# Performance work log

Measured on AMD Instinct MI355X. Metric: run time of the kernel, lower is better.

## Reference

```python
import jax, jax.numpy as jnp
import numpy as np
from jax import lax

# ---- fake-quant helpers (brevitas-style per-tensor float scaling, STE round) ----
EPS = 1e-8

def _ste_round(x):
    return x + lax.stop_gradient(jnp.round(x) - x)

def _scale(x, qmax):
    s = lax.stop_gradient(jnp.max(jnp.abs(x))) / qmax
    return jnp.maximum(s, EPS)

def fq(x, scale, qmin, qmax):
    # fake-quantize: round-to-nearest with straight-through estimator, clip, dequant
    return jnp.clip(_ste_round(x / scale), qmin, qmax) * scale

def quant_act_int8(x):
    s = _scale(x, 127.0)
    return fq(x, s, -128.0, 127.0), s

def quant_weight_int4(w):
    # 4-bit signed, narrow range [-7, 7] (brevitas weight quant default narrow_range)
    s = _scale(w, 7.0)
    return fq(w, s, -7.0, 7.0), s

def quant_relu_uint4(x):
    y = jax.nn.relu(x)
    s = _scale(y, 15.0)
    return fq(y, s, 0.0, 15.0)

def quant_bias_int32(b, scale):
    # Int32Bias: bias quantized at input_scale * weight_scale
    return _ste_round(b / scale) * scale

def conv2d_same(x, w):
    # NCHW, OIHW, padding=1, stride=1
    return lax.conv_general_dilated(x, w, window_strides=(1, 1), padding=((1, 1), (1, 1)),
                                    dimension_numbers=('NCHW', 'OIHW', 'NCHW'))

def maxpool2(x):
    return lax.reduce_window(x, -jnp.inf, lax.max, (1, 1, 2, 2), (1, 1, 2, 2), 'VALID')

def quant_conv(x, w, b):
    xq, sx = quant_act_int8(x)        # input_quant: Int8ActPerTensorFloat
    wq, sw = quant_weight_int4(w)     # weight_bit_width=4
    bq = quant_bias_int32(b, sx * sw) # bias_quant: Int32Bias
    y = conv2d_same(xq, wq) + bq[None, :, None, None]
    yq, _ = quant_act_int8(y)         # output_quant: Int8ActPerTensorFloat
    return yq

def quant_linear(x, w, b):
    xq, sx = quant_act_int8(x)
    wq, sw = quant_weight_int4(w)
    bq = quant_bias_int32(b, sx * sw)
    y = xq @ wq.T + bq
    yq, _ = quant_act_int8(y)
    return yq


def setup_inputs() -> dict:
    key = jax.random.key(0)
    ks = jax.random.split(key, 7)
    B = 8192
    x = jax.random.normal(ks[0], (B, 1, 28, 28), dtype=jnp.float32)
    w1 = jax.random.normal(ks[1], (16, 1, 3, 3), dtype=jnp.float32) * 0.3
    b1 = jax.random.normal(ks[2], (16,), dtype=jnp.float32) * 0.1
    w2 = jax.random.normal(ks[3], (32, 16, 3, 3), dtype=jnp.float32) * 0.1
    b2 = jax.random.normal(ks[4], (32,), dtype=jnp.float32) * 0.1
    wf = jax.random.normal(ks[5], (10, 32 * 7 * 7), dtype=jnp.float32) * 0.05
    bf = jax.random.normal(ks[6], (10,), dtype=jnp.float32) * 0.1
    return {'x': x, 'w1': w1, 'b1': b1, 'w2': w2, 'b2': b2, 'wf': wf, 'bf': bf}


def reference(x, w1, b1, w2, b2, wf, bf):
    h, _ = quant_act_int8(x)              # inputQuant
    h = quant_conv(h, w1, b1)             # conv1
    h = quant_relu_uint4(h)               # relu1 (4-bit)
    h = maxpool2(h)                       # pool1 -> [B,16,14,14]
    h = quant_conv(h, w2, b2)             # conv2
    h = quant_relu_uint4(h)               # relu2
    h = maxpool2(h)                       # pool2 -> [B,32,7,7]
    h = h.reshape(h.shape[0], -1)         # flatten -> [B,1568]
    return quant_linear(h, wf, bf)        # fc -> [B,10]
```

## Files before the change

### kernel.cpp

```cpp
#include <hip/hip_runtime.h>
#include <climits>

#define NB 8192
#define EPSQ 1e-8f

using i32x4  = __attribute__((ext_vector_type(4)))  int;
using i32x16 = __attribute__((ext_vector_type(16))) int;

#define WS_F(ws)     ((float*)(ws))
#define WS_I(ws)     ((int*)((char*)(ws)+128))
#define WS_B1L(ws)   ((int*)((char*)(ws)+384))
#define WS_B2L(ws)   ((int*)((char*)(ws)+448))
#define WS_BFL(ws)   ((int*)((char*)(ws)+576))
#define WS_M1F(ws)   ((float*)((char*)(ws)+640))
#define WS_B1F(ws)   ((float*)((char*)(ws)+1280))
#define WS_W1P(ws)   ((unsigned*)((char*)(ws)+1408))
#define WS_B2FR(ws)  ((char*)(ws)+2048)
#define WS_Q2TAB(ws) ((signed char*)((char*)(ws)+7168))
#define WS_Q3TAB(ws) ((signed char*)((char*)(ws)+7424))
#define WS_B1FR(ws)  ((char*)(ws)+7680)
#define WS_MFF(ws)   ((float*)((char*)(ws)+20480))
#define WS_WFP(ws)   ((char*)(ws)+83200)
#define WS_RA1(ws)   ((int*)((char*)(ws)+139264))
#define WS_RS1(ws)   ((int*)((char*)(ws)+164352))
#define WS_RA2(ws)   ((int*)((char*)(ws)+189440))
#define WS_RS2(ws)   ((int*)((char*)(ws)+197632))
#define WS_RA3(ws)   ((int*)((char*)(ws)+205824))
#define WS_RAX(ws)   ((float*)((char*)(ws)+206848))
#define WS_WMX(ws)   ((float*)((char*)(ws)+215040))
#define WS_Q2B(ws)   ((signed char*)((char*)(ws)+215552))
#define WS_BIG_OFF   281600

__device__ __forceinline__ float clampf(float v, float lo, float hi){ return fminf(fmaxf(v, lo), hi); }

__device__ __forceinline__ int dot4(unsigned a, unsigned b, int c){
  return __builtin_amdgcn_sdot4((int)a, (int)b, c, false);
}

__device__ __forceinline__ float wave_max_f(float v){
#pragma unroll
  for (int off=32; off; off>>=1) v = fmaxf(v, __shfl_down(v, off, 64));
  return v;
}
__device__ __forceinline__ int wave_max_i(int v){
#pragma unroll
  for (int off=32; off; off>>=1) v = max(v, __shfl_down(v, off, 64));
  return v;
}

__device__ __forceinline__ void reduce2_atomic(int amax, int smax, int* gA, int* gS){
  amax = wave_max_i(amax); smax = wave_max_i(smax);
  __shared__ int sA[4], sS[4];
  int w = threadIdx.x>>6, l = threadIdx.x&63;
  if (l==0){ sA[w]=amax; sS[w]=smax; }
  __syncthreads();
  if (threadIdx.x==0){
#pragma unroll
    for (int i=1;i<4;i++){ amax=max(amax,sA[i]); smax=max(smax,sS[i]); }
    atomicMax(gA, amax); atomicMax(gS, smax);
  }
}

__device__ __forceinline__ void reduce2_store(int amax, int smax, int* pA, int* pS){
  amax = wave_max_i(amax); smax = wave_max_i(smax);
  __shared__ int sA[4], sS[4];
  int w = threadIdx.x>>6, l = threadIdx.x&63;
  if (l==0){ sA[w]=amax; sS[w]=smax; }
  __syncthreads();
  if (threadIdx.x==0){
#pragma unroll
    for (int i=1;i<4;i++){ amax=max(amax,sA[i]); smax=max(smax,sS[i]); }
    *pA = amax; *pS = smax;
  }
}

__global__ void k_init(char* ws){
  int* I = WS_I(ws);
  if (threadIdx.x==0){ I[0]=0; I[1]=0; I[2]=INT_MIN; I[3]=0; I[4]=INT_MIN; I[5]=0; }
}

__global__ void k_absx(const float* __restrict__ x, char* ws){
  const float4* x4 = (const float4*)x;
  const int n4 = NB*784/4;
  float m = 0.f;
  for (int i = blockIdx.x*blockDim.x + threadIdx.x; i < n4; i += gridDim.x*blockDim.x){
    float4 v = x4[i];
    m = fmaxf(m, fmaxf(fmaxf(fabsf(v.x),fabsf(v.y)), fmaxf(fabsf(v.z),fabsf(v.w))));
  }
  m = wave_max_f(m);
  __shared__ float sm[4];
  int w = threadIdx.x>>6;
  if ((threadIdx.x&63)==0) sm[w]=m;
  __syncthreads();
  if (threadIdx.x==0){
    m = fmaxf(fmaxf(sm[0],sm[1]), fmaxf(sm[2],sm[3]));
    WS_RAX(ws)[blockIdx.x] = m;
  }
}

__global__ void k_absxw(const float* __restrict__ x,
                        const float* __restrict__ w1, const float* __restrict__ w2,
                        const float* __restrict__ wf, char* ws){
  __shared__ float red[256];
  int b = blockIdx.x, t = threadIdx.x;
  if (b < 81){
    float m = 0.f;
    if (b==0){ if (t<144) m = fabsf(w1[t]); }
    else if (b<19){ m = fabsf(w2[(b-1)*256 + t]); }
    else { int i=(b-19)*256+t; if (i<15680) m = fabsf(wf[i]); }
    red[t]=m; __syncthreads();
    for (int s=128;s;s>>=1){ if (t<s) red[t]=fmaxf(red[t],red[t+s]); __syncthreads(); }
    if (t==0) WS_WMX(ws)[b]=red[0];
    return;
  }
  const int xb = b - 81;
  const float4* x4 = (const float4*)x;
  const int n4 = NB*784/4;
  float m = 0.f;
  for (int i = xb*256 + t; i < n4; i += 2048*256){
    float4 v = x4[i];
    m = fmaxf(m, fmaxf(fmaxf(fabsf(v.x),fabsf(v.y)), fmaxf(fabsf(v.z),fabsf(v.w))));
  }
  m = wave_max_f(m);
  __shared__ float sm[4];
  int w = t>>6;
  if ((t&63)==0) sm[w]=m;
  __syncthreads();
  if (t==0){
    m = fmaxf(fmaxf(sm[0],sm[1]), fmaxf(sm[2],sm[3]));
    WS_RAX(ws)[xb] = m;
  }
}

__global__ void k_scales(const float* __restrict__ w1, const float* __restrict__ b1, char* ws){
  __shared__ float red[256];
  float* F = WS_F(ws);
  int t = threadIdx.x;
  float vw1 = WS_WMX(ws)[0];
  float m2=0.f, mf=0.f;
  if (t<18) m2 = WS_WMX(ws)[1+t];
  if (t<62) mf = WS_WMX(ws)[19+t];
  red[t]=m2; __syncthreads();
  for (int s=128;s;s>>=1){ if (t<s) red[t]=fmaxf(red[t],red[t+s]); __syncthreads(); }
  float mw2=red[0]; __syncthreads();
  red[t]=mf; __syncthreads();
  for (int s=128;s;s>>=1){ if (t<s) red[t]=fmaxf(red[t],red[t+s]); __syncthreads(); }
  float mwf=red[0]; __syncthreads();
  float mxv=0.f;
  for (int i=t;i<2048;i+=256) mxv=fmaxf(mxv,WS_RAX(ws)[i]);
  red[t]=mxv; __syncthreads();
  for (int s=128;s;s>>=1){ if (t<s) red[t]=fmaxf(red[t],red[t+s]); __syncthreads(); }
  float mx=red[0]; __syncthreads();

  float s0  = fmaxf(mx/127.f, EPSQ);
  float sx1 = fmaxf((127.f*s0)/127.f, EPSQ);
  float sw1 = fmaxf(vw1/7.f, EPSQ);
  float sw2 = fmaxf(mw2/7.f, EPSQ);
  float swf = fmaxf(mwf/7.f, EPSQ);
  float sb1 = sx1*sw1;
  if (t==0){ F[0]=s0; F[1]=sx1; F[2]=sw1; F[3]=sb1; F[7]=sw2; F[12]=swf; }
  if (t<144) WS_M1F(ws)[t] = clampf(rintf(w1[t]/sw1), -7.f, 7.f);
  if (t<16){
    int bl = (int)rintf(b1[t]/sb1);
    WS_B1L(ws)[t] = bl;
    WS_B1F(ws)[t] = (float)bl;
  }
  __syncthreads();
  if (t<48){
    int oc = t/3, row = t - oc*3;
    const float* m = WS_M1F(ws) + oc*9 + row*3;
    unsigned b0 = (unsigned)(unsigned char)(signed char)(int)m[0];
    unsigned bb1 = (unsigned)(unsigned char)(signed char)(int)m[1];
    unsigned b2c = (unsigned)(unsigned char)(signed char)(int)m[2];
    WS_W1P(ws)[t] = b0 | (bb1<<8) | (b2c<<16);
  }
}

__global__ void k_pack(const float* __restrict__ w1, const float* __restrict__ w2,
                       const float* __restrict__ wf, char* ws){
  const float* F = WS_F(ws);
  int id = blockIdx.x*256 + threadIdx.x;
  if (id < 5120){
    float sw2 = F[7];
    int chunk=id>>10, r=id&1023, ln=r>>4, j=r&15;
    int tap=2*chunk+(ln>>5), oc=ln&31;
    signed char v=0;
    if (tap<9) v=(signed char)clampf(rintf(w2[oc*144 + j*9 + tap]/sw2), -7.f, 7.f);
    WS_B2FR(ws)[id]=v;
  } else if (id < 6144){
    float sw1 = F[2];
    int i=id-5120;
    int ln=i>>4, j=i&15;
    int k=(ln>>5)*16+j, oc=ln&31;
    signed char v=0;
    if (k<9 && oc<16) v=(signed char)clampf(rintf(w1[oc*9+k]/sw1), -7.f, 7.f);
    WS_B1FR(ws)[i]=v;
  } else if (id < 56320){
    float swf = F[12];
    int i=id-6144;
    int chunk=i>>10, r2=i&1023, ln=r2>>4, j=r2&15;
    int oc=ln&31, k=chunk*32+(ln>>5)*16+j;
    int cell=k>>5, ch=k&31;
    signed char v=0;
    if (oc<10) v=(signed char)clampf(rintf(wf[oc*1568 + ch*49 + cell]/swf), -7.f, 7.f);
    ((signed char*)WS_WFP(ws))[i]=v;
  } else if (id < 72000){
    float swf = F[12];
    int i=id-56320;
    WS_MFF(ws)[i] = clampf(rintf(wf[i]/swf), -7.f, 7.f);
  }
}

__global__ void k_wq(const float* __restrict__ w1, const float* __restrict__ b1,
                     const float* __restrict__ w2, const float* __restrict__ wf,
                     char* ws){
  __shared__ float red[256];
  float* F = WS_F(ws);
  int t = threadIdx.x;
  auto bmaxabs = [&](const float* p, int n)->float{
    float m=0.f; for (int i=t;i<n;i+=256) m=fmaxf(m,fabsf(p[i]));
    red[t]=m; __syncthreads();
    for (int s=128;s;s>>=1){ if (t<s) red[t]=fmaxf(red[t],red[t+s]); __syncthreads(); }
    float r=red[0]; __syncthreads(); return r;
  };
  float mw1 = bmaxabs(w1,144);
  float mw2 = bmaxabs(w2,4608);
  float mwf = bmaxabs(wf,15680);
  float mxv=0.f;
  for (int i=t;i<2048;i+=256) mxv=fmaxf(mxv,WS_RAX(ws)[i]);
  red[t]=mxv; __syncthreads();
  for (int s=128;s;s>>=1){ if (t<s) red[t]=fmaxf(red[t],red[t+s]); __syncthreads(); }
  float mx=red[0]; __syncthreads();

  float s0  = fmaxf(mx/127.f, EPSQ);
  float sx1 = fmaxf((127.f*s0)/127.f, EPSQ);
  float sw1 = fmaxf(mw1/7.f, EPSQ);
  float sw2 = fmaxf(mw2/7.f, EPSQ);
  float swf = fmaxf(mwf/7.f, EPSQ);
  float sb1 = sx1*sw1;
  if (t==0){ F[0]=s0; F[1]=sx1; F[2]=sw1; F[3]=sb1; F[7]=sw2; F[12]=swf; }
  float* m1f = WS_M1F(ws);
  for (int i=t;i<144;i+=256) m1f[i] = clampf(rintf(w1[i]/sw1), -7.f, 7.f);
  if (t<16){
    int bl = (int)rintf(b1[t]/sb1);
    WS_B1L(ws)[t] = bl;
    WS_B1F(ws)[t] = (float)bl;
  }
  for (int i=t;i<5120;i+=256){
    int chunk=i>>10, r=i&1023, ln=r>>4, j=r&15;
    int tap=2*chunk+(ln>>5), oc=ln&31;
    signed char v=0;
    if (tap<9) v=(signed char)clampf(rintf(w2[oc*144 + j*9 + tap]/sw2), -7.f, 7.f);
    WS_B2FR(ws)[i]=v;
  }
  for (int i=t;i<1024;i+=256){
    int ln=i>>4, j=i&15;
    int k=(ln>>5)*16+j, oc=ln&31;
    signed char v=0;
    if (k<9 && oc<16) v=(signed char)clampf(rintf(w1[oc*9+k]/sw1), -7.f, 7.f);
    WS_B1FR(ws)[i]=v;
  }
  float* mff = WS_MFF(ws);
  for (int i=t;i<15680;i+=256) mff[i] = clampf(rintf(wf[i]/swf), -7.f, 7.f);
  for (int i=t;i<50176;i+=256){
    int chunk=i>>10, r2=i&1023, ln=r2>>4, j=r2&15;
    int oc=ln&31, k=chunk*32+(ln>>5)*16+j;
    int cell=k>>5, ch=k&31;
    signed char v=0;
    if (oc<10) v=(signed char)clampf(rintf(wf[oc*1568 + ch*49 + cell]/swf), -7.f, 7.f);
    ((signed char*)WS_WFP(ws))[i]=v;
  }
}

template<bool FULLR>
__global__ void k_s1(const float* __restrict__ b2, char* ws){
  float* F=WS_F(ws); int* I=WS_I(ws);
  __shared__ int rA[256], rS[256];
  __shared__ float sh[4];
  int t=threadIdx.x;
  int amaxI, smaxI;
  if constexpr (FULLR){
    int a=0, s=INT_MIN;
    const int* ra=WS_RA1(ws); const int* rs=WS_RS1(ws);
    for (int i=t;i<6272;i+=256){ a=max(a,ra[i]); s=max(s,rs[i]); }
    rA[t]=a; rS[t]=s; __syncthreads();
    for (int st=128;st;st>>=1){ if (t<st){ rA[t]=max(rA[t],rA[t+st]); rS[t]=max(rS[t],rS[t+st]); } __syncthreads(); }
    amaxI=rA[0]; smaxI=rS[0];
  } else { amaxI=I[1]; smaxI=I[2]; }
  if (t==0){
    float sb1=F[3];
    float sy1 = fmaxf((sb1*(float)amaxI)/127.f, EPSQ);
    float mp  = sb1*(float)smaxI;
    float P1  = clampf(rintf(mp/sy1), 0.f, 127.f);
    float sr1 = fmaxf((sy1*P1)/15.f, EPSQ);
    float N1  = clampf(rintf((sy1*P1)/sr1), 0.f, 15.f);
    float sx2 = fmaxf((N1*sr1)/127.f, EPSQ);
    float sb2 = sx2*F[7];
    F[4]=sy1; F[5]=sr1; F[6]=sx2; F[8]=sb2;
    sh[0]=sy1; sh[1]=sr1; sh[2]=sx2; sh[3]=sb2;
  }
  __syncthreads();
  float sy1=sh[0], sr1=sh[1], sx2=sh[2], sb2=sh[3];
  int k = t-128;
  float n = (k>0) ? clampf(rintf((sy1*(float)k)/sr1), 0.f, 15.f) : 0.f;
  WS_Q2TAB(ws)[t] = (signed char)clampf(rintf((n*sr1)/sx2), -128.f, 127.f);
  if (t<32) WS_B2L(ws)[t] = (int)rintf(b2[t]/sb2);
}

__global__ void k_s1q2(const float* __restrict__ b2, char* ws){
  float* F=WS_F(ws);
  __shared__ int rA[256], rS[256];
  int t=threadIdx.x;
  int a=0, s=INT_MIN;
  const int* ra=WS_RA1(ws); const int* rs=WS_RS1(ws);
  for (int i=t;i<6272;i+=256){ a=max(a,ra[i]); s=max(s,rs[i]); }
  rA[t]=a; rS[t]=s; __syncthreads();
  for (int st=128;st;st>>=1){ if (t<st){ rA[t]=max(rA[t],rA[t+st]); rS[t]=max(rS[t],rS[t+st]); } __syncthreads(); }
  int amaxI=rA[0], smaxI=rS[0];
  float sb1=F[3];
  float sy1 = fmaxf((sb1*(float)amaxI)/127.f, EPSQ);
  float P1  = clampf(rintf((sb1*(float)smaxI)/sy1), 0.f, 127.f);
  float sr1 = fmaxf((sy1*P1)/15.f, EPSQ);
  float N1  = clampf(rintf((sy1*P1)/sr1), 0.f, 15.f);
  float sx2 = fmaxf((N1*sr1)/127.f, EPSQ);
  float sb2 = sx2*F[7];
  if (blockIdx.x==0){
    if (t==0){ F[4]=sy1; F[5]=sr1; F[6]=sx2; F[8]=sb2; }
    if (t<32) WS_B2L(ws)[t] = (int)rintf(b2[t]/sb2);
  }
  int idx = blockIdx.x*256 + t;
  int m = idx - 32768;
  float k1 = clampf(rintf((sb1*(float)m)/sy1), -128.f, 127.f);
  float n  = (k1>0.f) ? clampf(rintf((sy1*k1)/sr1), 0.f, 15.f) : 0.f;
  WS_Q2B(ws)[idx] = (signed char)clampf(rintf((n*sr1)/sx2), -128.f, 127.f);
}

template<bool FULLR>
__global__ void k_s2(const float* __restrict__ bf, char* ws){
  float* F=WS_F(ws); int* I=WS_I(ws);
  __shared__ int rA[256], rS[256];
  __shared__ float sh[4];
  int t=threadIdx.x;
  int amaxI, smaxI;
  if constexpr (FULLR){
    int a=0, s=INT_MIN;
    const int* ra=WS_RA2(ws); const int* rs=WS_RS2(ws);
    for (int i=t;i<2048;i+=256){ a=max(a,ra[i]); s=max(s,rs[i]); }
    rA[t]=a; rS[t]=s; __syncthreads();
    for (int st=128;st;st>>=1){ if (t<st){ rA[t]=max(rA[t],rA[t+st]); rS[t]=max(rS[t],rS[t+st]); } __syncthreads(); }
    amaxI=rA[0]; smaxI=rS[0];
  } else { amaxI=I[3]; smaxI=I[4]; }
  if (t==0){
    float sb2=F[8];
    float sy2 = fmaxf((sb2*(float)amaxI)/127.f, EPSQ);
    float mp  = sb2*(float)smaxI;
    float P2  = clampf(rintf(mp/sy2), 0.f, 127.f);
    float sr2 = fmaxf((sy2*P2)/15.f, EPSQ);
    float N2  = clampf(rintf((sy2*P2)/sr2), 0.f, 15.f);
    float sx3 = fmaxf((N2*sr2)/127.f, EPSQ);
    float sb3 = sx3*F[12];
    F[9]=sy2; F[10]=sr2; F[11]=sx3; F[13]=sb3;
    sh[0]=sy2; sh[1]=sr2; sh[2]=sx3; sh[3]=sb3;
  }
  __syncthreads();
  float sy2=sh[0], sr2=sh[1], sx3=sh[2], sb3=sh[3];
  int k = t-128;
  float n = (k>0) ? clampf(rintf((sy2*(float)k)/sr2), 0.f, 15.f) : 0.f;
  WS_Q3TAB(ws)[t] = (signed char)clampf(rintf((n*sr2)/sx3), -128.f, 127.f);
  if (t<16) WS_BFL(ws)[t] = (t<10) ? (int)rintf(bf[t]/sb3) : 0;
}

template<bool FULLR>
__global__ void k_s3(char* ws){
  float* F=WS_F(ws); int* I=WS_I(ws);
  __shared__ int rA[256];
  int t=threadIdx.x;
  int amaxI;
  if constexpr (FULLR){
    rA[t] = WS_RA3(ws)[t];
    __syncthreads();
    for (int st=128;st;st>>=1){ if (t<st) rA[t]=max(rA[t],rA[t+st]); __syncthreads(); }
    amaxI = rA[0];
  } else { amaxI = I[5]; }
  if (t==0) F[14] = fmaxf((F[13]*(float)amaxI)/127.f, EPSQ);
}

__global__ void k_qx(const float* __restrict__ x, const char* __restrict__ ws,
                     signed char* __restrict__ qx){
  const float s0 = ((const float*)ws)[0];
  int id = blockIdx.x*256 + threadIdx.x;
  int img = id/240, w = id - img*240;
  int r = w>>3, c4 = (w&7)<<2;
  const float* xi = x + img*784;
  unsigned out = 0;
#pragma unroll
  for (int j=0;j<4;j++){
    int c = c4+j;
    bool valid = (r>=1) && (r<=28) && (c>=1) && (c<=28);
    int q = 0;
    if (valid){
      float xv = xi[(r-1)*28 + (c-1)];
      q = (int)clampf(rintf(xv/s0), -128.f, 127.f);
    }
    out |= ((unsigned)(unsigned char)(signed char)q) << (8*j);
  }
  ((unsigned*)qx)[id] = out;
}

__global__ __launch_bounds__(256) void k_conv1d(const signed char* __restrict__ qx,
                                                char* __restrict__ ws,
                                                short* __restrict__ i1p){
  const int t = threadIdx.x;
  const int id = blockIdx.x*256 + t;
  const int img = id/196, cell = id - img*196;
  const int py = cell/14, px = cell - py*14;
  const signed char* qb = qx + img*960 + (2*py)*32;
  const int pc0 = 2*px;
  const int al = pc0 & ~3, sh = (pc0&3)*8;
  unsigned wrd[4], whi[4];
#pragma unroll
  for (int rr=0; rr<4; rr++){
    unsigned lo = *(const unsigned*)(qb + rr*32 + al);
    unsigned hi = *(const unsigned*)(qb + rr*32 + al + 4);
    wrd[rr] = (unsigned)(((((unsigned long long)hi)<<32)|lo) >> sh);
    whi[rr] = wrd[rr] >> 8;
  }
  const unsigned* __restrict__ w1p = WS_W1P(ws);
  const int* __restrict__ b1l = WS_B1L(ws);
  int amax=0, smax=INT_MIN;
  short outv[16];
#pragma unroll
  for (int oc=0; oc<16; oc++){
    unsigned w0 = w1p[oc*3], w1 = w1p[oc*3+1], w2 = w1p[oc*3+2];
    int bl = b1l[oc];
    int a00 = dot4(wrd[2], w2, dot4(wrd[1], w1, dot4(wrd[0], w0, bl)));
    int a01 = dot4(whi[2], w2, dot4(whi[1], w1, dot4(whi[0], w0, bl)));
    int a10 = dot4(wrd[3], w2, dot4(wrd[2], w1, dot4(wrd[1], w0, bl)));
    int a11 = dot4(whi[3], w2, dot4(whi[2], w1, dot4(whi[1], w0, bl)));
    int mx = max(max(a00,a01), max(a10,a11));
    int ax = max(max(a00<0?-a00:a00, a01<0?-a01:a01), max(a10<0?-a10:a10, a11<0?-a11:a11));
    amax = max(amax, ax);
    smax = max(smax, mx);
    outv[oc] = (short)mx;
  }
  int4* dst = (int4*)(i1p + (size_t)id*16);
  dst[0] = *(const int4*)&outv[0];
  dst[1] = *(const int4*)&outv[8];
  reduce2_store(amax, smax, &WS_RA1(ws)[blockIdx.x], &WS_RS1(ws)[blockIdx.x]);
}

__global__ __launch_bounds__(256) void k_conv2r(char* __restrict__ ws,
                                                short* __restrict__ i1p,
                                                int* __restrict__ p2g){
  __shared__ __align__(16) signed char q2p4[4][4096];
  const int t=threadIdx.x, lane=t&63, wid=t>>6;
  const int img = blockIdx.x*4 + wid;
  signed char* q2p = q2p4[wid];
  const signed char* __restrict__ q2b = WS_Q2B(ws);

#pragma unroll
  for (int k=0;k<8;k++) ((unsigned long long*)q2p)[lane + 64*k] = 0ULL;

  const unsigned* src = (const unsigned*)(i1p + (size_t)img*3136);
#pragma unroll
  for (int k=0;k<24;k++){
    int idx = lane + 64*k;
    unsigned wv = src[idx];
    int e0 = idx*2;
    int cellc = e0 >> 4, ch = e0 & 15;
    int pyc = cellc/14, pxc = cellc - pyc*14;
    int m0 = (int)(short)(wv & 0xFFFFu);
    int m1 = (int)(short)(wv >> 16);
    int b0 = (int)(unsigned char)q2b[m0+32768];
    int b1 = (int)(unsigned char)q2b[m1+32768];
    *(unsigned short*)(q2p + ((pyc+1)*16 + (pxc+1))*16 + ch) = (unsigned short)(b0 | (b1<<8));
  }
  if (lane < 32){
    int idx = 1536 + lane;
    unsigned wv = src[idx];
    int e0 = idx*2;
    int cellc = e0 >> 4, ch = e0 & 15;
    int pyc = cellc/14, pxc = cellc - pyc*14;
    int m0 = (int)(short)(wv & 0xFFFFu);
    int m1 = (int)(short)(wv >> 16);
    int b0 = (int)(unsigned char)q2b[m0+32768];
    int b1 = (int)(unsigned char)q2b[m1+32768];
    *(unsigned short*)(q2p + ((pyc+1)*16 + (pxc+1))*16 + ch) = (unsigned short)(b0 | (b1<<8));
  }

  i32x4 bfr[5];
  const i32x4* bg = (const i32x4*)WS_B2FR(ws);
#pragma unroll
  for (int c=0;c<5;c++) bfr[c] = bg[c*64+lane];
  const int col = lane&31, h = lane>>5;
  const int bias = WS_B2L(ws)[col];
  int amax2=0, smax2=INT_MIN;
  const int TOFF[9] = {0,1,2,16,17,18,32,33,34};
  int* dstb = p2g + (size_t)img*1568;

#pragma unroll
  for (int mt=0; mt<7; mt++){
    int m = mt*32 + col;
    int g = m>>2, sub = m&3;
    bool gv = g < 49;
    int py = (g*37)>>8;
    int px = g - py*7;
    int oy = 2*py + (sub>>1), ox = 2*px + (sub&1);
    int E0 = oy*16 + ox;
    i32x16 acc;
#pragma unroll
    for (int r=0;r<16;r++) acc[r] = bias;
#pragma unroll
    for (int c=0;c<5;c++){
      const int t0 = TOFF[2*c];
      const int t1 = (2*c+1<9) ? TOFF[2*c+1] : -1;
      int toff = h ? t1 : t0;
      int entry = (gv && toff>=0) ? (E0 + toff) : 0;
      i32x4 a = *(const i32x4*)(q2p + entry*16);
      acc = __builtin_amdgcn_mfma_i32_32x32x32_i8(a, bfr[c], acc, 0,0,0);
    }
#pragma unroll
    for (int i=0;i<4;i++){
      int gg = mt*8 + 2*i + h;
      if (gg < 49){
        int v0=acc[4*i], v1=acc[4*i+1], v2=acc[4*i+2], v3=acc[4*i+3];
        int a0=v0<0?-v0:v0, a1=v1<0?-v1:v1, a2=v2<0?-v2:v2, a3=v3<0?-v3:v3;
        amax2 = max(amax2, max(max(a0,a1),max(a2,a3)));
        int mx = max(max(v0,v1),max(v2,v3));
        smax2 = max(smax2, mx);
        dstb[gg*32 + col] = mx;
      }
    }
  }
  reduce2_store(amax2, smax2, &WS_RA2(ws)[blockIdx.x], &WS_RS2(ws)[blockIdx.x]);
}

__global__ void k_rq2(const char* __restrict__ ws, const int* __restrict__ p2g,
                      signed char* __restrict__ q3g){
  const float* F = (const float*)ws;
  const float sb2 = F[8], sy2 = F[9];
  const signed char* q3t = WS_Q3TAB(ws);
  int id = blockIdx.x*256 + threadIdx.x;
  i32x4 m4 = ((const i32x4*)p2g)[id];
  unsigned out=0;
#pragma unroll
  for (int j=0;j<4;j++){
    float k2 = clampf(rintf((sb2*(float)m4[j])/sy2), -128.f, 127.f);
    out |= ((unsigned)(unsigned char)q3t[(int)k2+128]) << (8*j);
  }
  ((unsigned*)q3g)[id] = out;
}

__global__ __launch_bounds__(256) void k_fc(char* __restrict__ ws,
                                            const signed char* __restrict__ q3g,
                                            int* __restrict__ i3out){
  __shared__ int part[3][16][64];
  int t=threadIdx.x, lane=t&63, wid=t>>6;
  int mt = blockIdx.x;
  const int col=lane&31, h=lane>>5;
  const signed char* A0 = q3g + (size_t)(mt*32 + col)*1568 + 16*h;
  const i32x4* wfp = (const i32x4*)WS_WFP(ws);
  i32x16 acc;
#pragma unroll
  for (int r=0;r<16;r++) acc[r]=0;
#pragma unroll
  for (int cc=0; cc<13; cc++){
    int c = wid + cc*4;
    if (c < 49){
      i32x4 a = *(const i32x4*)(A0 + c*32);
      i32x4 b = wfp[c*64 + lane];
      acc = __builtin_amdgcn_mfma_i32_32x32x32_i8(a, b, acc, 0,0,0);
    }
  }
  if (wid>0){
#pragma unroll
    for (int r=0;r<16;r++) part[wid-1][r][lane] = acc[r];
  }
  __syncthreads();
  if (wid==0){
    int bias = (col<10) ? WS_BFL(ws)[col] : 0;
    int am=0;
#pragma unroll
    for (int r=0;r<16;r++){
      int v = acc[r] + part[0][r][lane] + part[1][r][lane] + part[2][r][lane] + bias;
      int row=(r&3)+8*(r>>2)+4*h;
      int img = mt*32+row;
      if (col<10){
        i3out[img*10+col] = v;
        am = max(am, v<0?-v:v);
      }
    }
    am = wave_max_i(am);
    if (lane==0) WS_RA3(ws)[blockIdx.x] = am;
  }
}

__global__ void k_out2(char* __restrict__ ws, float* __restrict__ out){
  __shared__ int rA[256];
  int t=threadIdx.x;
  rA[t] = WS_RA3(ws)[t];
  __syncthreads();
  for (int st=128;st;st>>=1){ if (t<st) rA[t]=max(rA[t],rA[t+st]); __syncthreads(); }
  float sb3 = WS_F(ws)[13];
  float sy3 = fmaxf((sb3*(float)rA[0])/127.f, EPSQ);
  int i = blockIdx.x*256 + t;
  if (i < NB*10){
    int iv = ((const int*)out)[i];
    float y = sb3*(float)iv;
    float q = clampf(rintf(y/sy3), -128.f, 127.f);
    out[i] = q*sy3;
  }
}

__global__ __launch_bounds__(256) void k_c1(const float* __restrict__ x, char* __restrict__ ws,
                                            short* __restrict__ i1p){
  constexpr int OFF_K0=0, OFF_A=960, OFF_I1=13760, OFF_B1=38848;
  __shared__ __align__(16) char arena[38912];
  signed char* k0b = (signed char*)(arena+OFF_K0);
  signed char* Abuf= (signed char*)(arena+OFF_A);
  short*       I1s = (short*)(arena+OFF_I1);
  int*         b1i = (int*)(arena+OFF_B1);

  const int tid=threadIdx.x, img=blockIdx.x;
  const int lane=tid&63, wid=tid>>6;
  const float s0 = WS_F(ws)[0];

  if (tid<16) b1i[tid]=WS_B1L(ws)[tid];
  for (int i=tid;i<240;i+=256) ((int*)k0b)[i]=0;
  for (int i=tid;i<3200;i+=256) ((int*)Abuf)[i]=0;
  __syncthreads();
  const float* xi = x + img*784;
  for (int i=tid;i<784;i+=256){
    int r=i/28, c=i-r*28;
    float v = clampf(rintf(xi[i]/s0), -128.f, 127.f);
    k0b[(r+1)*32 + (c+1)] = (signed char)v;
  }
  __syncthreads();
  for (int p=tid;p<784;p+=256){
    int oy=p/28, ox=p-oy*28;
    int base = oy*32+ox;
    int al = base & ~3, sh = (base&3)*8;
    unsigned l0a=*(const unsigned*)(k0b+al),    l1a=*(const unsigned*)(k0b+al+4);
    unsigned l0b=*(const unsigned*)(k0b+al+32), l1b=*(const unsigned*)(k0b+al+36);
    unsigned l0c=*(const unsigned*)(k0b+al+64), l1c=*(const unsigned*)(k0b+al+68);
    unsigned u0=(unsigned)(((((unsigned long long)l1a)<<32)|l0a)>>sh);
    unsigned u1=(unsigned)(((((unsigned long long)l1b)<<32)|l0b)>>sh);
    unsigned u2=(unsigned)(((((unsigned long long)l1c)<<32)|l0c)>>sh);
    i32x4 row;
    row[0]=(int)((u0&0xFFFFFFu)|(u1<<24));
    row[1]=(int)(((u1>>8)&0xFFFFu)|((u2&0xFFFFu)<<16));
    row[2]=(int)((u2>>16)&0xFFu);
    row[3]=0;
    *(i32x4*)(Abuf + p*16) = row;
  }
  __syncthreads();
  const i32x4 bfr = ((const i32x4*)WS_B1FR(ws))[lane];
  const int col=lane&31, h=lane>>5;
  const int bias=(col<16)? b1i[col] : 0;
  int amax=0, smax=INT_MIN;
  for (int mt=wid; mt<25; mt+=4){
    i32x4 a={0,0,0,0};
    if (h==0) a = *(const i32x4*)(Abuf + (mt*32+col)*16);
    i32x16 acc;
#pragma unroll
    for (int r=0;r<16;r++) acc[r]=bias;
    acc=__builtin_amdgcn_mfma_i32_32x32x32_i8(a,bfr,acc,0,0,0);
#pragma unroll
    for (int r=0;r<16;r++){
      int row=(r&3)+8*(r>>2)+4*h;
      int p=mt*32+row;
      if (p<784 && col<16){
        int v=acc[r];
        amax=max(amax,v<0?-v:v); smax=max(smax,v);
        I1s[p*16+col]=(short)v;
      }
    }
  }
  __syncthreads();
  for (int i=tid;i<3136;i+=256){
    int pp=i>>4, c=i&15, py=pp/14, px=pp-py*14;
    int p0=py*56+px*2;
    int m=max(max((int)I1s[p0*16+c],(int)I1s[(p0+1)*16+c]),
              max((int)I1s[(p0+28)*16+c],(int)I1s[(p0+29)*16+c]));
    i1p[(size_t)img*3136 + i]=(short)m;
  }
  reduce2_atomic(amax,smax,&WS_I(ws)[1],&WS_I(ws)[2]);
}

template<bool FIN>
__global__ __launch_bounds__(256) void k_c2(char* __restrict__ ws, const short* __restrict__ i1p,
                                            int* __restrict__ i3out){
  constexpr int OFF_Q2L=0, OFF_B2I=3136, OFF_Q2T=3264, OFF_N2=3520,
                OFF_Q3T=9792, OFF_BFS=10048, OFF_Q3F=10112, OFF_RED=16384;
  constexpr int ARENA = FIN ? 16544 : 3520;
  __shared__ __align__(16) char arena[ARENA];
  signed char* q2l=(signed char*)(arena+OFF_Q2L);
  int* b2li=(int*)(arena+OFF_B2I);
  signed char* q2t=(signed char*)(arena+OFF_Q2T);

  const int tid=threadIdx.x, img=blockIdx.x;
  const int lane=tid&63, wid=tid>>6;
  const float* F=WS_F(ws);
  const float sb1=F[3], sy1=F[4];

  q2t[tid]=WS_Q2TAB(ws)[tid];
  if (tid<32) b2li[tid]=WS_B2L(ws)[tid];
  if constexpr (FIN){
    ((signed char*)(arena+OFF_Q3T))[tid]=WS_Q3TAB(ws)[tid];
    if (tid<16) ((int*)(arena+OFF_BFS))[tid]=WS_BFL(ws)[tid];
  }
  __syncthreads();
  for (int i=tid;i<3136;i+=256){
    int m=(int)i1p[(size_t)img*3136+i];
    float k1=clampf(rintf((sb1*(float)m)/sy1),-128.f,127.f);
    q2l[i]=q2t[(int)k1+128];
  }
  __syncthreads();

  i32x4 bfr[5];
  {
    const i32x4* bg=(const i32x4*)WS_B2FR(ws);
#pragma unroll
    for (int c=0;c<5;c++) bfr[c]=bg[c*64+lane];
  }
  const int col=lane&31, h=lane>>5;
  const int bias=b2li[col];
  int amax2=0, smax2=INT_MIN;
  float sb2=0.f, sy2=0.f;
  signed char* n2buf=nullptr;
  if constexpr (FIN){ sb2=F[8]; sy2=F[9]; n2buf=(signed char*)(arena+OFF_N2); }

  for (int mt=wid; mt<7; mt+=4){
    const int p=mt*32+col;
    const bool pv=p<196;
    const int oy=p/14, ox=p-oy*14;
    i32x16 acc;
#pragma unroll
    for (int r=0;r<16;r++) acc[r]=bias;
#pragma unroll
    for (int c=0;c<5;c++){
      const int tap=2*c+h;
      i32x4 a={0,0,0,0};
      if (pv && tap<9){
        const int iy=oy+tap/3-1, ix=ox+tap-(tap/3)*3-1;
        if ((unsigned)iy<14u && (unsigned)ix<14u) a=*(const i32x4*)(q2l+(iy*14+ix)*16);
      }
      acc=__builtin_amdgcn_mfma_i32_32x32x32_i8(a,bfr[c],acc,0,0,0);
    }
#pragma unroll
    for (int r=0;r<16;r++){
      const int row=(r&3)+8*(r>>2)+4*h;
      const int pp=mt*32+row;
      if (pp<196){
        const int v=acc[r];
        if constexpr (!FIN){ amax2=max(amax2,v<0?-v:v); smax2=max(smax2,v); }
        else {
          n2buf[col*196+pp]=(signed char)clampf(rintf((sb2*(float)v)/sy2),-128.f,127.f);
        }
      }
    }
  }
  if constexpr (!FIN){
    reduce2_atomic(amax2,smax2,&WS_I(ws)[3],&WS_I(ws)[4]);
    return;
  } else {
    __syncthreads();
    signed char* q3t_s=(signed char*)(arena+OFF_Q3T);
    float* q3f=(float*)(arena+OFF_Q3F);
    for (int i=tid;i<1568;i+=256){
      int cch=i/49, s=i-cch*49, qy=s/7, qx=s-qy*7;
      int b=cch*196+qy*28+qx*2;
      int m=max(max((int)n2buf[b],(int)n2buf[b+1]),max((int)n2buf[b+14],(int)n2buf[b+15]));
      q3f[i]=(float)q3t_s[m+128];
    }
    __syncthreads();
    const float* mff=WS_MFF(ws);
    float a10[10];
#pragma unroll
    for (int o=0;o<10;o++) a10[o]=0.f;
    for (int k=tid;k<1568;k+=256){
      float qa=q3f[k];
#pragma unroll
      for (int o=0;o<10;o++) a10[o]=fmaf(qa,mff[o*1568+k],a10[o]);
    }
#pragma unroll
    for (int o=0;o<10;o++){
#pragma unroll
      for (int off=32;off;off>>=1) a10[o]+=__shfl_down(a10[o],off,64);
    }
    float* redf=(float*)(arena+OFF_RED);
    int* bfs=(int*)(arena+OFF_BFS);
    if (lane==0){
#pragma unroll
      for (int o=0;o<10;o++) redf[wid*10+o]=a10[o];
    }
    __syncthreads();
    if (tid<10){
      float s=redf[tid]+redf[10+tid]+redf[20+tid]+redf[30+tid];
      int I3v=(int)s+bfs[tid];
      i3out[img*10+tid]=I3v;
      redf[tid]=(float)(I3v<0?-I3v:I3v);
    }
    __syncthreads();
    if (tid==0){
      int m=0;
#pragma unroll
      for (int o=0;o<10;o++) m=max(m,(int)redf[o]);
      atomicMax(&WS_I(ws)[5],m);
    }
  }
}

__global__ void k_out(char* ws, float* __restrict__ out){
  float* F=WS_F(ws);
  float sb3=F[13], sy3=F[14];
  int i = blockIdx.x*blockDim.x + threadIdx.x;
  if (i < NB*10){
    int iv = ((const int*)out)[i];
    float y = sb3*(float)iv;
    float q = clampf(rintf(y/sy3), -128.f, 127.f);
    out[i] = q*sy3;
  }
}

extern "C" void kernel_launch(void* const* d_in, const int* in_sizes, int n_in,
                              void* d_out, int out_size, void* d_ws, size_t ws_size,
                              hipStream_t stream){
  const float* x  = (const float*)d_in[0];
  const float* w1 = (const float*)d_in[1];
  const float* b1 = (const float*)d_in[2];
  const float* w2 = (const float*)d_in[3];
  const float* b2 = (const float*)d_in[4];
  const float* wf = (const float*)d_in[5];
  const float* bf = (const float*)d_in[6];
  char* ws = (char*)d_ws;
  float* out = (float*)d_out;
  int* i3 = (int*)d_out;

  const size_t QX_SZ  = (size_t)NB*960;
  const size_t I1_SZ  = (size_t)NB*6272;
  const size_t Q3_SZ  = (size_t)NB*1568;
  const size_t needFull = (size_t)WS_BIG_OFF + QX_SZ + I1_SZ + Q3_SZ;

  if (ws_size >= needFull){
    signed char* qx  = (signed char*)(ws + WS_BIG_OFF);
    short*       i1p = (short*)(ws + WS_BIG_OFF + QX_SZ);
    int*         p2g = (int*)i1p;
    signed char* q3g = (signed char*)(ws + WS_BIG_OFF + QX_SZ + I1_SZ);
    k_absxw <<<dim3(2129), dim3(256), 0, stream>>>(x, w1, w2, wf, ws);
    k_scales<<<dim3(1), dim3(256), 0, stream>>>(w1, b1, ws);
    k_qx    <<<dim3(NB*240/256), dim3(256), 0, stream>>>(x, ws, qx);
    k_pack  <<<dim3(282), dim3(256), 0, stream>>>(w1, w2, wf, ws);
    k_conv1d<<<dim3(NB*196/256), dim3(256), 0, stream>>>(qx, ws, i1p);
    k_s1q2  <<<dim3(256), dim3(256), 0, stream>>>(b2, ws);
    k_conv2r<<<dim3(NB/4), dim3(256), 0, stream>>>(ws, i1p, p2g);
    k_s2<true><<<dim3(1), dim3(256), 0, stream>>>(bf, ws);
    k_rq2   <<<dim3(NB*1568/1024), dim3(256), 0, stream>>>(ws, p2g, q3g);
    k_fc    <<<dim3(256), dim3(256), 0, stream>>>(ws, q3g, i3);
    k_out2  <<<dim3((NB*10+255)/256), dim3(256), 0, stream>>>(ws, out);
  } else {
    short* i1p = (short*)(ws + WS_BIG_OFF);
    k_init<<<dim3(1), dim3(64), 0, stream>>>(ws);
    k_absx<<<dim3(2048), dim3(256), 0, stream>>>(x, ws);
    k_wq  <<<dim3(1), dim3(256), 0, stream>>>(w1, b1, w2, wf, ws);
    k_c1<<<dim3(NB), dim3(256), 0, stream>>>(x, ws, i1p);
    k_s1<false><<<dim3(1), dim3(256), 0, stream>>>(b2, ws);
    k_c2<false><<<dim3(NB), dim3(256), 0, stream>>>(ws, i1p, i3);
    k_s2<false><<<dim3(1), dim3(256), 0, stream>>>(bf, ws);
    k_c2<true ><<<dim3(NB), dim3(256), 0, stream>>>(ws, i1p, i3);
    k_s3<false><<<dim3(1), dim3(256), 0, stream>>>(ws);
    k_out<<<dim3((NB*10+255)/256), dim3(256), 0, stream>>>(ws, out);
  }
}
```

Measured before the change: 118.8 us.

## Fold single-block scale kernels into consumer grids, redundantly recomputing reductions per block

```diff
diff --git a/kernel.cpp b/kernel.cpp
--- a/kernel.cpp
+++ b/kernel.cpp
@@ -132,83 +132,115 @@
   }
 }
 
-__global__ void k_scales(const float* __restrict__ w1, const float* __restrict__ b1, char* ws){
-  __shared__ float red[256];
-  float* F = WS_F(ws);
+__device__ __forceinline__ float red_wmx_range(char* ws, int lo, int n, float* red){
   int t = threadIdx.x;
-  float vw1 = WS_WMX(ws)[0];
-  float m2=0.f, mf=0.f;
-  if (t<18) m2 = WS_WMX(ws)[1+t];
-  if (t<62) mf = WS_WMX(ws)[19+t];
-  red[t]=m2; __syncthreads();
+  float m=0.f;
+  if (t<n) m = WS_WMX(ws)[lo+t];
+  red[t]=m; __syncthreads();
   for (int s=128;s;s>>=1){ if (t<s) red[t]=fmaxf(red[t],red[t+s]); __syncthreads(); }
-  float mw2=red[0]; __syncthreads();
-  red[t]=mf; __syncthreads();
-  for (int s=128;s;s>>=1){ if (t<s) red[t]=fmaxf(red[t],red[t+s]); __syncthreads(); }
-  float mwf=red[0]; __syncthreads();
+  float r=red[0]; __syncthreads();
+  return r;
+}
+__device__ __forceinline__ float red_rax(char* ws, float* red){
+  int t = threadIdx.x;
   float mxv=0.f;
   for (int i=t;i<2048;i+=256) mxv=fmaxf(mxv,WS_RAX(ws)[i]);
   red[t]=mxv; __syncthreads();
   for (int s=128;s;s>>=1){ if (t<s) red[t]=fmaxf(red[t],red[t+s]); __syncthreads(); }
-  float mx=red[0]; __syncthreads();
-
-  float s0  = fmaxf(mx/127.f, EPSQ);
-  float sx1 = fmaxf((127.f*s0)/127.f, EPSQ);
-  float sw1 = fmaxf(vw1/7.f, EPSQ);
-  float sw2 = fmaxf(mw2/7.f, EPSQ);
-  float swf = fmaxf(mwf/7.f, EPSQ);
-  float sb1 = sx1*sw1;
-  if (t==0){ F[0]=s0; F[1]=sx1; F[2]=sw1; F[3]=sb1; F[7]=sw2; F[12]=swf; }
-  if (t<144) WS_M1F(ws)[t] = clampf(rintf(w1[t]/sw1), -7.f, 7.f);
-  if (t<16){
-    int bl = (int)rintf(b1[t]/sb1);
-    WS_B1L(ws)[t] = bl;
-    WS_B1F(ws)[t] = (float)bl;
-  }
-  __syncthreads();
-  if (t<48){
-    int oc = t/3, row = t - oc*3;
-    const float* m = WS_M1F(ws) + oc*9 + row*3;
-    unsigned b0 = (unsigned)(unsigned char)(signed char)(int)m[0];
-    unsigned bb1 = (unsigned)(unsigned char)(signed char)(int)m[1];
-    unsigned b2c = (unsigned)(unsigned char)(signed char)(int)m[2];
-    WS_W1P(ws)[t] = b0 | (bb1<<8) | (b2c<<16);
-  }
-}
-
-__global__ void k_pack(const float* __restrict__ w1, const float* __restrict__ w2,
-                       const float* __restrict__ wf, char* ws){
-  const float* F = WS_F(ws);
-  int id = blockIdx.x*256 + threadIdx.x;
-  if (id < 5120){
-    float sw2 = F[7];
-    int chunk=id>>10, r=id&1023, ln=r>>4, j=r&15;
-    int tap=2*chunk+(ln>>5), oc=ln&31;
-    signed char v=0;
-    if (tap<9) v=(signed char)clampf(rintf(w2[oc*144 + j*9 + tap]/sw2), -7.f, 7.f);
-    WS_B2FR(ws)[id]=v;
-  } else if (id < 6144){
-    float sw1 = F[2];
-    int i=id-5120;
-    int ln=i>>4, j=i&15;
-    int k=(ln>>5)*16+j, oc=ln&31;
-    signed char v=0;
-    if (k<9 && oc<16) v=(signed char)clampf(rintf(w1[oc*9+k]/sw1), -7.f, 7.f);
-    WS_B1FR(ws)[i]=v;
-  } else if (id < 56320){
-    float swf = F[12];
-    int i=id-6144;
-    int chunk=i>>10, r2=i&1023, ln=r2>>4, j=r2&15;
-    int oc=ln&31, k=chunk*32+(ln>>5)*16+j;
-    int cell=k>>5, ch=k&31;
-    signed char v=0;
-    if (oc<10) v=(signed char)clampf(rintf(wf[oc*1568 + ch*49 + cell]/swf), -7.f, 7.f);
-    ((signed char*)WS_WFP(ws))[i]=v;
-  } else if (id < 72000){
-    float swf = F[12];
-    int i=id-56320;
-    WS_MFF(ws)[i] = clampf(rintf(wf[i]/swf), -7.f, 7.f);
-  }
+  float r=red[0]; __syncthreads();
+  return r;
+}
+
+__global__ void k_prep(const float* __restrict__ x,
+                       const float* __restrict__ w1, const float* __restrict__ b1,
+                       const float* __restrict__ w2, const float* __restrict__ wf,
+                       char* __restrict__ ws, signed char* __restrict__ qx){
+  __shared__ float red[256];
+  const int b = blockIdx.x, t = threadIdx.x;
+  if (b == 0){
+    float vw1 = WS_WMX(ws)[0];
+    float mw2 = red_wmx_range(ws, 1, 18, red);
+    float mwf = red_wmx_range(ws, 19, 62, red);
+    float mx  = red_rax(ws, red);
+    float* F = WS_F(ws);
+    float s0  = fmaxf(mx/127.f, EPSQ);
+    float sx1 = fmaxf((127.f*s0)/127.f, EPSQ);
+    float sw1 = fmaxf(vw1/7.f, EPSQ);
+    float sw2 = fmaxf(mw2/7.f, EPSQ);
+    float swf = fmaxf(mwf/7.f, EPSQ);
+    float sb1 = sx1*sw1;
+    if (t==0){ F[0]=s0; F[1]=sx1; F[2]=sw1; F[3]=sb1; F[7]=sw2; F[12]=swf; }
+    if (t<144) WS_M1F(ws)[t] = clampf(rintf(w1[t]/sw1), -7.f, 7.f);
+    if (t<16){
+      int bl = (int)rintf(b1[t]/sb1);
+      WS_B1L(ws)[t] = bl;
+      WS_B1F(ws)[t] = (float)bl;
+    }
+    __syncthreads();
+    if (t<48){
+      int oc = t/3, row = t - oc*3;
+      const float* m = WS_M1F(ws) + oc*9 + row*3;
+      unsigned b0 = (unsigned)(unsigned char)(signed char)(int)m[0];
+      unsigned bb1 = (unsigned)(unsigned char)(signed char)(int)m[1];
+      unsigned b2c = (unsigned)(unsigned char)(signed char)(int)m[2];
+      WS_W1P(ws)[t] = b0 | (bb1<<8) | (b2c<<16);
+    }
+    return;
+  }
+  if (b < 283){
+    float vw1 = WS_WMX(ws)[0];
+    float mw2 = red_wmx_range(ws, 1, 18, red);
+    float mwf = red_wmx_range(ws, 19, 62, red);
+    float sw1 = fmaxf(vw1/7.f, EPSQ);
+    float sw2 = fmaxf(mw2/7.f, EPSQ);
+    float swf = fmaxf(mwf/7.f, EPSQ);
+    int id = (b-1)*256 + t;
+    if (id < 5120){
+      int chunk=id>>10, r=id&1023, ln=r>>4, j=r&15;
+      int tap=2*chunk+(ln>>5), oc=ln&31;
+      signed char v=0;
+      if (tap<9) v=(signed char)clampf(rintf(w2[oc*144 + j*9 + tap]/sw2), -7.f, 7.f);
+      WS_B2FR(ws)[id]=v;
+    } else if (id < 6144){
+      int i=id-5120;
+      int ln=i>>4, j=i&15;
+      int k=(ln>>5)*16+j, oc=ln&31;
+      signed char v=0;
+      if (k<9 && oc<16) v=(signed char)clampf(rintf(w1[oc*9+k]/sw1), -7.f, 7.f);
+      WS_B1FR(ws)[i]=v;
+    } else if (id < 56320){
+      int i=id-6144;
+      int chunk=i>>10, r2=i&1023, ln=r2>>4, j=r2&15;
+      int oc=ln&31, k=chunk*32+(ln>>5)*16+j;
+      int cell=k>>5, ch=k&31;
+      signed char v=0;
+      if (oc<10) v=(signed char)clampf(rintf(wf[oc*1568 + ch*49 + cell]/swf), -7.f, 7.f);
+      ((signed char*)WS_WFP(ws))[i]=v;
+    } else if (id < 72000){
+      int i=id-56320;
+      WS_MFF(ws)[i] = clampf(rintf(wf[i]/swf), -7.f, 7.f);
+    }
+    return;
+  }
+  float mx = red_rax(ws, red);
+  float s0 = fmaxf(mx/127.f, EPSQ);
+  int id = (b-283)*256 + t;
+  int img = id/240, w = id - img*240;
+  int r = w>>3, c4 = (w&7)<<2;
+  const float* xi = x + img*784;
+  unsigned out = 0;
+#pragma unroll
+  for (int j=0;j<4;j++){
+    int c = c4+j;
+    bool valid = (r>=1) && (r<=28) && (c>=1) && (c<=28);
+    int q = 0;
+    if (valid){
+      float xv = xi[(r-1)*28 + (c-1)];
+      q = (int)clampf(rintf(xv/s0), -128.f, 127.f);
+    }
+    out |= ((unsigned)(unsigned char)(signed char)q) << (8*j);
+  }
+  ((unsigned*)qx)[id] = out;
 }
 
 __global__ void k_wq(const float* __restrict__ w1, const float* __restrict__ b1,
@@ -385,28 +417,6 @@
   if (t==0) F[14] = fmaxf((F[13]*(float)amaxI)/127.f, EPSQ);
 }
 
-__global__ void k_qx(const float* __restrict__ x, const char* __restrict__ ws,
-                     signed char* __restrict__ qx){
-  const float s0 = ((const float*)ws)[0];
-  int id = blockIdx.x*256 + threadIdx.x;
-  int img = id/240, w = id - img*240;
-  int r = w>>3, c4 = (w&7)<<2;
-  const float* xi = x + img*784;
-  unsigned out = 0;
-#pragma unroll
-  for (int j=0;j<4;j++){
-    int c = c4+j;
-    bool valid = (r>=1) && (r<=28) && (c>=1) && (c<=28);
-    int q = 0;
-    if (valid){
-      float xv = xi[(r-1)*28 + (c-1)];
-      q = (int)clampf(rintf(xv/s0), -128.f, 127.f);
-    }
-    out |= ((unsigned)(unsigned char)(signed char)q) << (8*j);
-  }
-  ((unsigned*)qx)[id] = out;
-}
-
 __global__ __launch_bounds__(256) void k_conv1d(const signed char* __restrict__ qx,
                                                 char* __restrict__ ws,
                                                 short* __restrict__ i1p){
@@ -535,12 +545,36 @@
   reduce2_store(amax2, smax2, &WS_RA2(ws)[blockIdx.x], &WS_RS2(ws)[blockIdx.x]);
 }
 
-__global__ void k_rq2(const char* __restrict__ ws, const int* __restrict__ p2g,
-                      signed char* __restrict__ q3g){
-  const float* F = (const float*)ws;
-  const float sb2 = F[8], sy2 = F[9];
-  const signed char* q3t = WS_Q3TAB(ws);
-  int id = blockIdx.x*256 + threadIdx.x;
+__global__ void k_rq2s(const float* __restrict__ bf, char* __restrict__ ws,
+                       const int* __restrict__ p2g, signed char* __restrict__ q3g){
+  float* F = WS_F(ws);
+  __shared__ int rA[256], rS[256];
+  __shared__ signed char q3t[256];
+  int t=threadIdx.x;
+  int a=0, s=INT_MIN;
+  const int* ra=WS_RA2(ws); const int* rs=WS_RS2(ws);
+  for (int i=t;i<2048;i+=256){ a=max(a,ra[i]); s=max(s,rs[i]); }
+  rA[t]=a; rS[t]=s; __syncthreads();
+  for (int st=128;st;st>>=1){ if (t<st){ rA[t]=max(rA[t],rA[t+st]); rS[t]=max(rS[t],rS[t+st]); } __syncthreads(); }
+  int amaxI=rA[0], smaxI=rS[0];
+  float sb2=F[8];
+  float sy2 = fmaxf((sb2*(float)amaxI)/127.f, EPSQ);
+  float P2  = clampf(rintf((sb2*(float)smaxI)/sy2), 0.f, 127.f);
+  float sr2 = fmaxf((sy2*P2)/15.f, EPSQ);
+  float N2  = clampf(rintf((sy2*P2)/sr2), 0.f, 15.f);
+  float sx3 = fmaxf((N2*sr2)/127.f, EPSQ);
+  float sb3 = sx3*F[12];
+  if (blockIdx.x==0){
+    if (t==0){ F[9]=sy2; F[10]=sr2; F[11]=sx3; F[13]=sb3; }
+    if (t<16) WS_BFL(ws)[t] = (t<10) ? (int)rintf(bf[t]/sb3) : 0;
+  }
+  {
+    int k = t-128;
+    float n = (k>0) ? clampf(rintf((sy2*(float)k)/sr2), 0.f, 15.f) : 0.f;
+    q3t[t] = (signed char)clampf(rintf((n*sr2)/sx3), -128.f, 127.f);
+  }
+  __syncthreads();
+  int id = blockIdx.x*256 + t;
   i32x4 m4 = ((const i32x4*)p2g)[id];
   unsigned out=0;
 #pragma unroll
@@ -848,14 +882,11 @@
     int*         p2g = (int*)i1p;
     signed char* q3g = (signed char*)(ws + WS_BIG_OFF + QX_SZ + I1_SZ);
     k_absxw <<<dim3(2129), dim3(256), 0, stream>>>(x, w1, w2, wf, ws);
-    k_scales<<<dim3(1), dim3(256), 0, stream>>>(w1, b1, ws);
-    k_qx    <<<dim3(NB*240/256), dim3(256), 0, stream>>>(x, ws, qx);
-    k_pack  <<<dim3(282), dim3(256), 0, stream>>>(w1, w2, wf, ws);
+    k_prep  <<<dim3(283 + NB*240/256), dim3(256), 0, stream>>>(x, w1, b1, w2, wf, ws, qx);
     k_conv1d<<<dim3(NB*196/256), dim3(256), 0, stream>>>(qx, ws, i1p);
     k_s1q2  <<<dim3(256), dim3(256), 0, stream>>>(b2, ws);
     k_conv2r<<<dim3(NB/4), dim3(256), 0, stream>>>(ws, i1p, p2g);
-    k_s2<true><<<dim3(1), dim3(256), 0, stream>>>(bf, ws);
-    k_rq2   <<<dim3(NB*1568/1024), dim3(256), 0, stream>>>(ws, p2g, q3g);
+    k_rq2s  <<<dim3(NB*1568/1024), dim3(256), 0, stream>>>(bf, ws, p2g, q3g);
     k_fc    <<<dim3(256), dim3(256), 0, stream>>>(ws, q3g, i3);
     k_out2  <<<dim3((NB*10+255)/256), dim3(256), 0, stream>>>(ws, out);
   } else {
```

Result: slower. 124.4 us (+4.7%).
